# Kernel optimization log

Measured on AMD Instinct MI355X. Metric: run time of the kernel, lower is better.

The kernel has to match this reference:

```python
import jax, jax.numpy as jnp
import numpy as np

B, CIN, COUT, G, HEADS = 4, 256, 256, 8, 4
K, S, P = 7, 1, 3
H = W = 32
IN_W = CIN // G
OUT_W = COUT // G


def setup_inputs() -> dict:
    key = jax.random.key(0)
    ks = jax.random.split(key, 9)
    def n(k, shape, scale=1.0):
        return jax.random.normal(k, shape, dtype=jnp.float32) * scale
    # kaiming fan_out init for the 1x1 convs (fan_out = out channels)
    return {
        "x": n(ks[0], (B, CIN, H, W)),
        "wq": n(ks[1], (G, OUT_W * HEADS, IN_W), (2.0 / (OUT_W * HEADS)) ** 0.5),
        "bq": n(ks[2], (G, OUT_W * HEADS), 0.01),
        "wk": n(ks[3], (G, OUT_W, IN_W), (2.0 / OUT_W) ** 0.5),
        "bk": n(ks[4], (G, OUT_W), 0.01),
        "wv": n(ks[5], (G, OUT_W, IN_W), (2.0 / OUT_W) ** 0.5),
        "bv": n(ks[6], (G, OUT_W), 0.01),
        "rel_h": n(ks[7], (OUT_W // 2, 1, 1, G, K, 1)),
        "rel_w": n(ks[8], (OUT_W // 2, 1, 1, G, 1, K)),
    }


def _sparse_conv(x, w, b):
    # grouped 1x1 conv, groups stacked on last axis (matches torch.stack(dim=-1))
    # x: [B, G*I, h, w]; w: [G, O, I]; b: [G, O] -> [B, O, h, w, G]
    Bn, C, hh, ww = x.shape
    xr = x.reshape(Bn, G, C // G, hh, ww)
    out = jnp.einsum('bgihw,goi->bohwg', xr, w)
    return out + b.T[None, :, None, None, :]


def _unfold(x5, k, s):
    # x5: [B, C, Hp, Wp, G] -> [B, C, Ho, Wo, G, k, k]  (torch unfold(2).unfold(3))
    Bn, C, Hp, Wp, Gn = x5.shape
    Ho = (Hp - k) // s + 1
    Wo = (Wp - k) // s + 1
    patches = jnp.stack(
        [x5[:, :, i:i + (Ho - 1) * s + 1:s, j:j + (Wo - 1) * s + 1:s, :]
         for i in range(k) for j in range(k)], axis=-1)
    return patches.reshape(Bn, C, Ho, Wo, Gn, k, k)


def reference(x, wq, bq, wk, bk, wv, bv, rel_h, rel_w):
    xp = jnp.pad(x, ((0, 0), (0, 0), (P, P), (P, P)))
    q = _sparse_conv(x, wq, bq)    # [B, OUT_W*HEADS, H, W, G]
    k = _sparse_conv(xp, wk, bk)   # [B, OUT_W, Hp, Wp, G] (bias at padded locations, as in torch)
    v = _sparse_conv(xp, wv, bv)
    k = _unfold(k, K, S)           # [B, OUT_W, H, W, G, K, K]
    v = _unfold(v, K, S)
    kh, kw = jnp.split(k, 2, axis=1)
    k = jnp.concatenate([kh + rel_h, kw + rel_w], axis=1)
    kf = k.reshape(B, OUT_W, H, W, G * K * K)
    vf = v.reshape(B, OUT_W, H, W, G * K * K)
    q = q.reshape(B, HEADS, OUT_W, H, W, G)
    # scores: sum over channel c; softmax over flattened (group, kh, kw) window
    scores = jnp.einsum('bhcxyg,bcxym->bhxygm', q, kf)
    attn = jax.nn.softmax(scores, axis=-1)
    # weighted sum over window m and heads h (matches sum(dim=1) then sum(dim=-1))
    out = jnp.einsum('bhxygm,bcxym->bcxyg', attn, vf)   # [B, OUT_W, H, W, G]
    out = jnp.transpose(out, (0, 4, 2, 3, 1)).reshape(B, -1, H, W)  # transpose(1,-1)+reshape
    return out
```

## Files before the change

kernel.cpp:

```cpp
#include <hip/hip_runtime.h>
#include <math.h>

typedef _Float16 f16;
typedef _Float16 f16x8 __attribute__((ext_vector_type(8)));
typedef __bf16 bf16x8 __attribute__((ext_vector_type(8)));
typedef __bf16 bf16x8a4 __attribute__((ext_vector_type(8), aligned(4)));
typedef float f32x4 __attribute__((ext_vector_type(4)));

#define MFMA_F16(a, b, c)  __builtin_amdgcn_mfma_f32_16x16x32_f16(a, b, c, 0, 0, 0)
#define MFMA_BF16(a, b, c) __builtin_amdgcn_mfma_f32_16x16x32_bf16(a, b, c, 0, 0, 0)

__global__ __launch_bounds__(256) void produce_kernel(
    const float* __restrict__ x,
    const float* __restrict__ wq, const float* __restrict__ bq,
    const float* __restrict__ wk, const float* __restrict__ bk,
    const float* __restrict__ wv, const float* __restrict__ bv,
    const float* __restrict__ rel_h, const float* __restrict__ rel_w,
    f16* __restrict__ Qb, f16* __restrict__ Kb,
    __bf16* __restrict__ VtA, __bf16* __restrict__ VtB,
    f16* __restrict__ relp) {
    int bid = blockIdx.x;
    int t = threadIdx.x;

    if (bid == 1216) {
        for (int idx = t; idx < 448 * 32; idx += 256) {
            int c = idx & 31, key = idx >> 5;
            int kw = key & 7, ghk = key >> 3;
            int gp = (ghk * 37) >> 8;
            int kh = ghk - gp * 7;
            float v = 0.f;
            if (kw < 7)
                v = (c < 16) ? rel_h[c * 56 + gp * 7 + kh]
                             : rel_w[(c - 16) * 56 + gp * 7 + kw];
            relp[idx] = (f16)v;
        }
        return;
    }

    int hp = bid % 38, g = (bid / 38) & 7, b = bid / 304;
    bool hin = (hp >= 3 && hp < 35);
    size_t kvbase = (size_t)(b * 8 + g);

    if (!hin) {
        for (int idx = t; idx < 38 * 32; idx += 256) {
            int wp = idx >> 5, c = idx & 31;
            Kb[((kvbase * 38 + hp) * 38 + wp) * 32 + c] = (f16)bk[g * 32 + c];
        }
        for (int idx = t; idx < 40 * 32; idx += 256) {
            int i = idx >> 5, c = idx & 31;
            size_t vo = ((kvbase * 32 + c) * 38 + hp) * 40;
            __bf16 bb = (__bf16)bv[g * 32 + c];
            VtA[vo + i] = (i < 38) ? bb : (__bf16)0.f;
            VtB[vo + i] = (i < 37) ? bb : (__bf16)0.f;
        }
        return;
    }

    int h = hp - 3;
    __shared__ __align__(16) f16 xTl[32 * 40];

    {
        int ic = t >> 3, w = (t & 7) * 4;
        float4 xv = *(const float4*)(x + (((size_t)b * 256 + g * 32 + ic) * 32 + h) * 32 + w);
        xTl[(w + 0) * 40 + ic] = (f16)xv.x;
        xTl[(w + 1) * 40 + ic] = (f16)xv.y;
        xTl[(w + 2) * 40 + ic] = (f16)xv.z;
        xTl[(w + 3) * 40 + ic] = (f16)xv.w;
    }
    __syncthreads();

    int l15 = t & 15, quad = (t >> 4) & 3, wave = t >> 6;

    f16x8 a0 = *(const f16x8*)(xTl + l15 * 40 + quad * 8);
    f16x8 a1 = *(const f16x8*)(xTl + (16 + l15) * 40 + quad * 8);

#pragma unroll
    for (int i = 0; i < 2; ++i) {
        int Nt = wave * 2 + i;
        const float4* wp4 = (const float4*)(wq + ((size_t)g * 128 + Nt * 16 + l15) * 32 + quad * 8);
        float4 u0 = wp4[0], u1 = wp4[1];
        f16x8 bfrag;
        bfrag[0] = (f16)u0.x; bfrag[1] = (f16)u0.y; bfrag[2] = (f16)u0.z; bfrag[3] = (f16)u0.w;
        bfrag[4] = (f16)u1.x; bfrag[5] = (f16)u1.y; bfrag[6] = (f16)u1.z; bfrag[7] = (f16)u1.w;
        float bias = bq[g * 128 + Nt * 16 + l15];
#pragma unroll
        for (int Mt = 0; Mt < 2; ++Mt) {
            f32x4 d = {0.f, 0.f, 0.f, 0.f};
            d = MFMA_F16(Mt ? a1 : a0, bfrag, d);
#pragma unroll
            for (int r = 0; r < 4; ++r) {
                int w = Mt * 16 + quad * 4 + r;
                Qb[(size_t)((b * 32 + h) * 32 + w) * 1024 + g * 128 + Nt * 16 + l15] =
                    (f16)(d[r] + bias);
            }
        }
    }

    {
        int sel = wave & 1, Nth = wave >> 1;
        const float* wsrc = sel ? wv : wk;
        const float4* wp4 = (const float4*)(wsrc + ((size_t)g * 32 + Nth * 16 + l15) * 32 + quad * 8);
        float4 u0 = wp4[0], u1 = wp4[1];
        f16x8 bfrag;
        bfrag[0] = (f16)u0.x; bfrag[1] = (f16)u0.y; bfrag[2] = (f16)u0.z; bfrag[3] = (f16)u0.w;
        bfrag[4] = (f16)u1.x; bfrag[5] = (f16)u1.y; bfrag[6] = (f16)u1.z; bfrag[7] = (f16)u1.w;
        float bias = (sel ? bv : bk)[g * 32 + Nth * 16 + l15];
        int c = Nth * 16 + l15;
#pragma unroll
        for (int Mt = 0; Mt < 2; ++Mt) {
            f32x4 d = {0.f, 0.f, 0.f, 0.f};
            d = MFMA_F16(Mt ? a1 : a0, bfrag, d);
#pragma unroll
            for (int r = 0; r < 4; ++r) {
                int wp = Mt * 16 + quad * 4 + r + 3;
                float v = d[r] + bias;
                if (!sel) {
                    Kb[((kvbase * 38 + hp) * 38 + wp) * 32 + c] = (f16)v;
                } else {
                    size_t vo = ((kvbase * 32 + c) * 38 + hp) * 40;
                    VtA[vo + wp] = (__bf16)v;
                    VtB[vo + wp - 1] = (__bf16)v;
                }
            }
        }
    }

    for (int idx = t; idx < 192; idx += 256) {
        int wi = idx >> 5, c = idx & 31;
        int wp = (wi < 3) ? wi : (32 + wi);
        Kb[((kvbase * 38 + hp) * 38 + wp) * 32 + c] = (f16)bk[g * 32 + c];
        size_t vo = ((kvbase * 32 + c) * 38 + hp) * 40;
        __bf16 bb = (__bf16)bv[g * 32 + c];
        VtA[vo + wp] = bb;
        if (wp >= 1) VtB[vo + wp - 1] = bb;
    }
    for (int idx = t; idx < 160; idx += 256) {
        int c = idx / 5, j = idx % 5;
        size_t vo = ((kvbase * 32 + c) * 38 + hp) * 40;
        if (j < 2) VtA[vo + 38 + j] = (__bf16)0.f;
        else       VtB[vo + 35 + j] = (__bf16)0.f;
    }
}

__global__ __launch_bounds__(64, 4) void attn_kernel(
    const f16* __restrict__ Qb, const f16* __restrict__ Kb,
    const __bf16* __restrict__ VtA, const __bf16* __restrict__ VtB,
    const f16* __restrict__ relp, float* __restrict__ out) {
    int bid = blockIdx.x;
    int pid = (bid & 7) * 512 + (bid >> 3);
    int y = pid & 31, x = (pid >> 5) & 31, b = pid >> 10;

    __shared__ __align__(16) __bf16 Pl[32 * 136];

    int t = threadIdx.x;
    int l15 = t & 15, quad = t >> 4, kwl = t & 7, p8 = (t >> 3) & 1;
    bool mask7 = (kwl == 7);

    {
        int row = t >> 1, off = 112 + (t & 1) * 8;
        *(uint4*)(Pl + row * 136 + off) = (uint4){0u, 0u, 0u, 0u};
    }

    f16x8 qf[2];
    {
        const f16* qp = Qb + (size_t)pid * 1024;
        qf[0] = *(const f16x8*)(qp + l15 * 32 + quad * 8);
        qf[1] = *(const f16x8*)(qp + (16 + l15) * 32 + quad * 8);
    }

    float fsum[2][4];
#pragma unroll
    for (int m = 0; m < 2; ++m)
#pragma unroll
        for (int r = 0; r < 4; ++r) fsum[m][r] = 0.f;

    f32x4 acc[2][2];
#pragma unroll
    for (int m = 0; m < 2; ++m)
#pragma unroll
        for (int n = 0; n < 2; ++n) acc[m][n] = (f32x4){0.f, 0.f, 0.f, 0.f};

    int yk = y + kwl;
    if (yk > 37) yk = 37;
    const __bf16* __restrict__ Vsel = (y & 1) ? VtB : VtA;
    int yv = y & ~1;

    for (int chunk = 0; chunk < 4; ++chunk) {
        int gp = chunk * 2 + p8;
        const f16* kbp = Kb + ((((size_t)(b * 8 + gp) * 38 + x) * 38 + yk) << 5) + quad * 8;
        const f16* rpp = relp + (size_t)(gp * 7 * 8 + kwl) * 32 + quad * 8;
#pragma unroll
        for (int kh = 0; kh < 7; ++kh) {
            f16x8 kb = *(const f16x8*)kbp;
            f16x8 rp = *(const f16x8*)rpp;
            kbp += 38 * 32;
            rpp += 256;
            kb += rp;
#pragma unroll
            for (int Mt = 0; Mt < 2; ++Mt) {
                f32x4 d = {0.f, 0.f, 0.f, 0.f};
                d = MFMA_F16(qf[Mt], kb, d);
#pragma unroll
                for (int r = 0; r < 4; ++r) {
                    float e = __expf(d[r]);
                    e = mask7 ? 0.f : e;
                    fsum[Mt][r] += e;
                    Pl[(Mt * 16 + quad * 4 + r) * 136 + kh * 16 + l15] = (__bf16)e;
                }
            }
        }

        int gpv = chunk * 2 + (quad & 1);
        int qh = quad >> 1;
#pragma unroll
        for (int ks = 0; ks < 4; ++ks) {
            bf16x8 af0 = *(const bf16x8*)(Pl + l15 * 136 + ks * 32 + quad * 8);
            bf16x8 af1 = *(const bf16x8*)(Pl + (16 + l15) * 136 + ks * 32 + quad * 8);
            int kh = 2 * ks + qh;
            int khc = (kh > 6) ? 6 : kh;
#pragma unroll
            for (int t2 = 0; t2 < 2; ++t2) {
                const __bf16* vp =
                    Vsel + (((size_t)(b * 8 + gpv) * 32 + t2 * 16 + l15) * 38 + x + khc) * 40 + yv;
                bf16x8a4 bv8 = *(const bf16x8a4*)vp;
                acc[0][t2] = MFMA_BF16(af0, (bf16x8)bv8, acc[0][t2]);
                acc[1][t2] = MFMA_BF16(af1, (bf16x8)bv8, acc[1][t2]);
            }
        }
    }

#pragma unroll
    for (int dlt = 1; dlt < 16; dlt <<= 1)
#pragma unroll
        for (int m = 0; m < 2; ++m)
#pragma unroll
            for (int r = 0; r < 4; ++r) fsum[m][r] += __shfl_xor(fsum[m][r], dlt);

    float inv[2][4];
#pragma unroll
    for (int m = 0; m < 2; ++m)
#pragma unroll
        for (int r = 0; r < 4; ++r) inv[m][r] = 1.0f / fsum[m][r];

#pragma unroll
    for (int Mt = 0; Mt < 2; ++Mt)
#pragma unroll
        for (int t2 = 0; t2 < 2; ++t2) {
            float o = 0.f;
#pragma unroll
            for (int r = 0; r < 4; ++r) o = fmaf(acc[Mt][t2][r], inv[Mt][r], o);
            int g = Mt * 4 + quad;
            out[(((size_t)(b * 8 + g) * 32 + x) * 32 + y) * 32 + t2 * 16 + l15] = o;
        }
}

extern "C" void kernel_launch(void* const* d_in, const int* in_sizes, int n_in,
                              void* d_out, int out_size, void* d_ws, size_t ws_size,
                              hipStream_t stream) {
    const float* x     = (const float*)d_in[0];
    const float* wq    = (const float*)d_in[1];
    const float* bq    = (const float*)d_in[2];
    const float* wk    = (const float*)d_in[3];
    const float* bk    = (const float*)d_in[4];
    const float* wv    = (const float*)d_in[5];
    const float* bv    = (const float*)d_in[6];
    const float* rel_h = (const float*)d_in[7];
    const float* rel_w = (const float*)d_in[8];
    float* out = (float*)d_out;

    unsigned char* ws = (unsigned char*)d_ws;
    f16*    Qb   = (f16*)ws;
    f16*    Kb   = (f16*)(ws + 8388608);
    __bf16* VtA  = (__bf16*)(ws + 8388608 + 2957312);
    __bf16* VtB  = (__bf16*)(ws + 8388608 + 2957312 + 3112960);
    f16*    relp = (f16*)(ws + 8388608 + 2957312 + 3112960 + 3112960);

    hipLaunchKernelGGL(produce_kernel, dim3(1217), dim3(256), 0, stream,
                       x, wq, bq, wk, bk, wv, bv, rel_h, rel_w, Qb, Kb, VtA, VtB, relp);
    hipLaunchKernelGGL(attn_kernel, dim3(4096), dim3(64), 0, stream,
                       Qb, Kb, VtA, VtB, relp, out);
}
```

Baseline: 126.6 us.

## Compute softmax denominator with MFMA ones-vector and pack two pixels per block

The per-lane exp sum and its cross-lane shuffle reduction are replaced by an extra bf16 MFMA against a ones vector that sums each probability row, and the mask is enforced by zeroing the eighth V element instead of zeroing the exp. The exp input is clamped to avoid overflow. Blocks now hold two wavefronts (two pixels) with separate LDS tiles, halving the grid size. This cuts VALU adds and shuffles at the cost of extra MFMAs, and the row sum is now taken from bf16-rounded probabilities, which may change numerics slightly.

```diff
diff --git a/kernel.cpp b/kernel.cpp
--- a/kernel.cpp
+++ b/kernel.cpp
@@ -142,23 +142,26 @@
     }
 }
 
-__global__ __launch_bounds__(64, 4) void attn_kernel(
+__global__ __launch_bounds__(128, 4) void attn_kernel(
     const f16* __restrict__ Qb, const f16* __restrict__ Kb,
     const __bf16* __restrict__ VtA, const __bf16* __restrict__ VtB,
     const f16* __restrict__ relp, float* __restrict__ out) {
     int bid = blockIdx.x;
-    int pid = (bid & 7) * 512 + (bid >> 3);
+    int t = threadIdx.x;
+    int wv = t >> 6;
+    int pb = (bid & 7) * 256 + (bid >> 3);
+    int pid = pb * 2 + wv;
     int y = pid & 31, x = (pid >> 5) & 31, b = pid >> 10;
 
-    __shared__ __align__(16) __bf16 Pl[32 * 136];
-
-    int t = threadIdx.x;
-    int l15 = t & 15, quad = t >> 4, kwl = t & 7, p8 = (t >> 3) & 1;
-    bool mask7 = (kwl == 7);
-
-    {
-        int row = t >> 1, off = 112 + (t & 1) * 8;
-        *(uint4*)(Pl + row * 136 + off) = (uint4){0u, 0u, 0u, 0u};
+    __shared__ __align__(16) __bf16 Pl[2 * 32 * 136];
+    __bf16* Plw = Pl + wv * (32 * 136);
+
+    int lane = t & 63;
+    int l15 = t & 15, quad = (t >> 4) & 3, kwl = t & 7;
+
+    {
+        int row = lane >> 1, off = 112 + (lane & 1) * 8;
+        *(uint4*)(Plw + row * 136 + off) = (uint4){0u, 0u, 0u, 0u};
     }
 
     f16x8 qf[2];
@@ -168,17 +171,22 @@
         qf[1] = *(const f16x8*)(qp + (16 + l15) * 32 + quad * 8);
     }
 
-    float fsum[2][4];
-#pragma unroll
-    for (int m = 0; m < 2; ++m)
-#pragma unroll
-        for (int r = 0; r < 4; ++r) fsum[m][r] = 0.f;
+    bf16x8 onesf;
+    {
+        __bf16 v = (l15 == 0) ? (__bf16)1.0f : (__bf16)0.0f;
+#pragma unroll
+        for (int j = 0; j < 7; ++j) onesf[j] = v;
+        onesf[7] = (__bf16)0.0f;
+    }
 
     f32x4 acc[2][2];
-#pragma unroll
-    for (int m = 0; m < 2; ++m)
+    f32x4 acc2[2];
+#pragma unroll
+    for (int m = 0; m < 2; ++m) {
+        acc2[m] = (f32x4){0.f, 0.f, 0.f, 0.f};
 #pragma unroll
         for (int n = 0; n < 2; ++n) acc[m][n] = (f32x4){0.f, 0.f, 0.f, 0.f};
+    }
 
     int yk = y + kwl;
     if (yk > 37) yk = 37;
@@ -186,7 +194,7 @@
     int yv = y & ~1;
 
     for (int chunk = 0; chunk < 4; ++chunk) {
-        int gp = chunk * 2 + p8;
+        int gp = chunk * 2 + ((t >> 3) & 1);
         const f16* kbp = Kb + ((((size_t)(b * 8 + gp) * 38 + x) * 38 + yk) << 5) + quad * 8;
         const f16* rpp = relp + (size_t)(gp * 7 * 8 + kwl) * 32 + quad * 8;
 #pragma unroll
@@ -202,10 +210,8 @@
                 d = MFMA_F16(qf[Mt], kb, d);
 #pragma unroll
                 for (int r = 0; r < 4; ++r) {
-                    float e = __expf(d[r]);
-                    e = mask7 ? 0.f : e;
-                    fsum[Mt][r] += e;
-                    Pl[(Mt * 16 + quad * 4 + r) * 136 + kh * 16 + l15] = (__bf16)e;
+                    float e = __expf(fminf(d[r], 80.f));
+                    Plw[(Mt * 16 + quad * 4 + r) * 136 + kh * 16 + l15] = (__bf16)e;
                 }
             }
         }
@@ -214,8 +220,8 @@
         int qh = quad >> 1;
 #pragma unroll
         for (int ks = 0; ks < 4; ++ks) {
-            bf16x8 af0 = *(const bf16x8*)(Pl + l15 * 136 + ks * 32 + quad * 8);
-            bf16x8 af1 = *(const bf16x8*)(Pl + (16 + l15) * 136 + ks * 32 + quad * 8);
+            bf16x8 af0 = *(const bf16x8*)(Plw + l15 * 136 + ks * 32 + quad * 8);
+            bf16x8 af1 = *(const bf16x8*)(Plw + (16 + l15) * 136 + ks * 32 + quad * 8);
             int kh = 2 * ks + qh;
             int khc = (kh > 6) ? 6 : kh;
 #pragma unroll
@@ -223,24 +229,21 @@
                 const __bf16* vp =
                     Vsel + (((size_t)(b * 8 + gpv) * 32 + t2 * 16 + l15) * 38 + x + khc) * 40 + yv;
                 bf16x8a4 bv8 = *(const bf16x8a4*)vp;
+                bv8[7] = (__bf16)0.0f;
                 acc[0][t2] = MFMA_BF16(af0, (bf16x8)bv8, acc[0][t2]);
                 acc[1][t2] = MFMA_BF16(af1, (bf16x8)bv8, acc[1][t2]);
             }
-        }
-    }
-
-#pragma unroll
-    for (int dlt = 1; dlt < 16; dlt <<= 1)
-#pragma unroll
-        for (int m = 0; m < 2; ++m)
-#pragma unroll
-            for (int r = 0; r < 4; ++r) fsum[m][r] += __shfl_xor(fsum[m][r], dlt);
+            acc2[0] = MFMA_BF16(af0, onesf, acc2[0]);
+            acc2[1] = MFMA_BF16(af1, onesf, acc2[1]);
+        }
+    }
 
     float inv[2][4];
 #pragma unroll
     for (int m = 0; m < 2; ++m)
 #pragma unroll
-        for (int r = 0; r < 4; ++r) inv[m][r] = 1.0f / fsum[m][r];
+        for (int r = 0; r < 4; ++r)
+            inv[m][r] = 1.0f / __shfl(acc2[m][r], t & 48);
 
 #pragma unroll
     for (int Mt = 0; Mt < 2; ++Mt)
@@ -277,6 +280,6 @@
 
     hipLaunchKernelGGL(produce_kernel, dim3(1217), dim3(256), 0, stream,
                        x, wq, bq, wk, bk, wv, bv, rel_h, rel_w, Qb, Kb, VtA, VtB, relp);
-    hipLaunchKernelGGL(attn_kernel, dim3(4096), dim3(64), 0, stream,
+    hipLaunchKernelGGL(attn_kernel, dim3(2048), dim3(128), 0, stream,
                        Qb, Kb, VtA, VtB, relp, out);
 }
```

Result: slower. 130.5 us (+3.1%).
